# Kernel tuning notes

Hardware: AMD Instinct MI355X
Metric: run time of the kernel (lower is better)

The kernel has to match this reference:

```python
import jax, jax.numpy as jnp
import numpy as np

SAMPLE_POINTS = 1000
THRESH = 0.1
MAX_RATIO = 0.1
BIG = 1e9


def _sobel_boundary(mask):
    # mask: [B, H, W] -> boundary magnitude [B, H, W]
    kx = jnp.array([[-1, 0, 1], [-2, 0, 2], [-1, 0, 1]], jnp.float32).reshape(1, 1, 3, 3)
    ky = jnp.array([[-1, -2, -1], [0, 0, 0], [1, 2, 1]], jnp.float32).reshape(1, 1, 3, 3)
    x = mask[:, None, :, :]
    dn = ('NCHW', 'OIHW', 'NCHW')
    gx = jax.lax.conv_general_dilated(x, kx, (1, 1), [(1, 1), (1, 1)], dimension_numbers=dn)
    gy = jax.lax.conv_general_dilated(x, ky, (1, 1), [(1, 1), (1, 1)], dimension_numbers=dn)
    return jnp.sqrt(gx * gx + gy * gy + 1e-8)[:, 0]


def _extract_points(bmap, keys, H, W):
    # bmap: [B, H, W]. Returns points [B, P, 2] float and validity mask [B, P].
    # Torch version uses torch.where + randperm subsampling; here we pick a
    # uniformly-random subset of valid boundary pixels via noisy top_k
    # (fixed-shape, jit-compatible stream compaction).
    def one(bm, key):
        flat = bm.reshape(-1)
        valid = flat > THRESH
        noise = jax.random.uniform(key, flat.shape)
        score = valid.astype(jnp.float32) * 2.0 + noise  # valid in (2,3), invalid in (0,1)
        _, idx = jax.lax.top_k(score, SAMPLE_POINTS)
        pts = jnp.stack([(idx // W).astype(jnp.float32), (idx % W).astype(jnp.float32)], axis=-1)
        pvalid = valid[idx]
        has_any = valid.any()
        # empty-boundary fallback: single center point (like torch version)
        center = jnp.array([H // 2, W // 2], jnp.float32)
        pts = jnp.where(has_any, pts, jnp.broadcast_to(center, pts.shape))
        pvalid = jnp.where(has_any, pvalid, jnp.arange(SAMPLE_POINTS) == 0)
        return pts, pvalid

    return jax.vmap(one)(bmap, keys)


def _hausdorff(pp, pv, tp, tv, diag):
    # pp: [B,P,2], tp: [B,T,2]; masked symmetric Hausdorff per batch element.
    pp2 = jnp.sum(pp * pp, -1)  # [B,P]
    tp2 = jnp.sum(tp * tp, -1)  # [B,T]
    d2 = pp2[:, :, None] + tp2[:, None, :] - 2.0 * jnp.einsum('bpc,btc->bpt', pp, tp)
    D = jnp.sqrt(jnp.maximum(d2, 0.0))  # [B,P,T]
    min_p2t = jnp.min(jnp.where(tv[:, None, :], D, BIG), axis=2)  # [B,P]
    a = jnp.max(jnp.where(pv, min_p2t, -BIG), axis=1)  # [B]
    min_t2p = jnp.min(jnp.where(pv[:, :, None], D, BIG), axis=1)  # [B,T]
    b = jnp.max(jnp.where(tv, min_t2p, -BIG), axis=1)  # [B]
    hd = jnp.maximum(a, b) / diag
    return jnp.clip(hd, 0.0, MAX_RATIO)


def setup_inputs() -> dict:
    key = jax.random.key(0)
    k1, k2 = jax.random.split(key)
    B, H, W = 64, 512, 512
    pred_logits = jax.random.normal(k1, (B, H, W), dtype=jnp.float32)
    target = (jax.random.uniform(k2, (B, H, W)) > 0.5).astype(jnp.float32)
    return {"pred_logits": pred_logits, "target": target}


def reference(pred_logits, target):
    B, H, W = pred_logits.shape
    pred_probs = jax.nn.sigmoid(pred_logits)
    bmap_pred = _sobel_boundary(pred_probs)
    bmap_tgt = _sobel_boundary(target)
    keys = jax.random.split(jax.random.key(1), 2 * B)
    pp, pv = _extract_points(bmap_pred, keys[:B], H, W)
    tp, tv = _extract_points(bmap_tgt, keys[B:], H, W)
    diag = jnp.sqrt(jnp.float32(H * H + W * W))
    hd = _hausdorff(pp, pv, tp, tv, diag)  # [B]
    return jnp.mean(hd)
```

## Files before the change

### kernel.cpp

```cpp
#include <hip/hip_runtime.h>
#include <stdint.h>


#define HH 512
#define WW 512
#define NPIX (HH * WW)
#define NSEL 1000
#define SLICE_CAP 320
#define CUTM (253u << 14)
#define BITCUT ((((253u << 15) - 1u)) << 9)
#define ROWS_PER 32

#if __has_builtin(__builtin_amdgcn_alignbit)
__device__ __forceinline__ uint32_t rotl32(uint32_t x, int r) {
  return __builtin_amdgcn_alignbit(x, x, (32 - r) & 31);
}
#else
__device__ __forceinline__ uint32_t rotl32(uint32_t x, int r) {
  return (x << r) | (x >> (32 - r));
}
#endif

__device__ __forceinline__ void tf2x32(uint32_t k0, uint32_t k1,
                                       uint32_t c0, uint32_t c1,
                                       uint32_t& o0, uint32_t& o1) {
  uint32_t ks2 = k0 ^ k1 ^ 0x1BD11BDAu;
  uint32_t x0 = c0 + k0, x1 = c1 + k1;
#define TF_R(r) { x0 += x1; x1 = rotl32(x1, (r)); x1 ^= x0; }
  TF_R(13) TF_R(15) TF_R(26) TF_R(6)
  x0 += k1;  x1 += ks2 + 1u;
  TF_R(17) TF_R(29) TF_R(16) TF_R(24)
  x0 += ks2; x1 += k0 + 2u;
  TF_R(13) TF_R(15) TF_R(26) TF_R(6)
  x0 += k0;  x1 += k1 + 3u;
  TF_R(17) TF_R(29) TF_R(16) TF_R(24)
  x0 += k1;  x1 += ks2 + 4u;
  TF_R(13) TF_R(15) TF_R(26) TF_R(6)
  x0 += ks2; x1 += k0 + 5u;
#undef TF_R
  o0 = x0; o1 = x1;
}

__device__ __forceinline__ uint32_t tf_bits(uint32_t k0, uint32_t k1, uint32_t p) {
  uint32_t ks2 = k0 ^ k1 ^ 0x1BD11BDAu;
  uint32_t x0 = k0, x1 = p + k1;
#define TF_R(r) { x0 += x1; x1 = rotl32(x1, (r)); x1 ^= x0; }
  TF_R(13) TF_R(15) TF_R(26) TF_R(6)
  x0 += k1;  x1 += ks2 + 1u;
  TF_R(17) TF_R(29) TF_R(16) TF_R(24)
  x0 += ks2; x1 += k0 + 2u;
  TF_R(13) TF_R(15) TF_R(26) TF_R(6)
  x0 += k0;  x1 += k1 + 3u;
  TF_R(17) TF_R(29) TF_R(16) TF_R(24)
  x0 += k1;  x1 += ks2 + 4u;
  TF_R(13) TF_R(15) TF_R(26) TF_R(6)
  x0 += ks2; x1 += k0 + 5u;
#undef TF_R
  return x0 ^ x1;
}

__device__ __forceinline__ uint32_t m_from_bits(uint32_t bits) {
  float noise = __uint_as_float((bits >> 9) | 0x3F800000u) - 1.0f;
  float score = 2.0f + noise;
  return __float_as_uint(score) - 0x40000000u;
}

__device__ __forceinline__ uint32_t pixel_m(uint32_t k0, uint32_t k1, int p) {
  uint32_t b1, b2;
  tf2x32(k0, k1, 0u, (uint32_t)p, b1, b2);
  return m_from_bits(b1 ^ b2);
}

__device__ __forceinline__ float sigf(float x) { return 1.0f / (1.0f + __expf(-x)); }

__device__ __forceinline__ float ldval(const float* __restrict__ img, int r, int c, bool isPred) {
  if (r < 0 || r > HH - 1 || c < 0 || c > WW - 1) return 0.0f;
  float v = img[(size_t)r * WW + c];
  return isPred ? sigf(v) : v;
}

__device__ __forceinline__ uint32_t pack_pt(uint32_t p) {
  return ((p >> 9) << 16) | (p & 511u);
}

template <bool PRED>
__device__ __forceinline__ void sobel_body(const float* __restrict__ img, int b,
                                           int slice, int t,
                                           unsigned long long* stage, int* s_cn,
                                           int* s_cv) {
  const int lane = t & 63, w = t >> 6;
  const int rbase = slice * ROWS_PER + 8 * w;
  uint32_t k0, k1;
  tf2x32(0u, 1u, 0u, (uint32_t)b, k0, k1);
  k0 = __builtin_amdgcn_readfirstlane(k0);
  k1 = __builtin_amdgcn_readfirstlane(k1);

  float4 ra[3], rb[3];
  float v[3][10];
  int cnt = 0;
  const uint32_t pbase = (uint32_t)((rbase << 9) + (lane << 3));

  auto load_raw = [&](int s, int rn) {
    if ((unsigned)rn < (unsigned)HH) {
      const float* rp = img + ((size_t)rn << 9) + (lane << 3);
      ra[s] = *(const float4*)rp;
      rb[s] = *(const float4*)(rp + 4);
    }
  };
  auto promote = [&](int s, int rn) {
    float (&vv)[10] = v[s];
    if ((unsigned)rn < (unsigned)HH) {
      float4 x = ra[s], y = rb[s];
      if (PRED) {
        x.x = sigf(x.x); x.y = sigf(x.y); x.z = sigf(x.z); x.w = sigf(x.w);
        y.x = sigf(y.x); y.y = sigf(y.y); y.z = sigf(y.z); y.w = sigf(y.w);
      }
      vv[1] = x.x; vv[2] = x.y; vv[3] = x.z; vv[4] = x.w;
      vv[5] = y.x; vv[6] = y.y; vv[7] = y.z; vv[8] = y.w;
      float l = __shfl_up(y.w, 1);
      float r = __shfl_down(x.x, 1);
      vv[0] = (lane == 0) ? 0.0f : l;
      vv[9] = (lane == 63) ? 0.0f : r;
    } else {
#pragma unroll
      for (int i = 0; i < 10; ++i) vv[i] = 0.0f;
    }
  };

  load_raw(0, rbase - 1);
  load_raw(1, rbase);
  load_raw(2, rbase + 1);
  promote(0, rbase - 1);
  promote(1, rbase);

#pragma unroll
  for (int r = 0; r < 8; ++r) {
    load_raw(r % 3, rbase + r + 2);

    const uint32_t prow_r = pbase + (uint32_t)(r << 9);
    uint32_t bits[8];
#pragma unroll
    for (int j = 0; j < 8; ++j) bits[j] = tf_bits(k0, k1, prow_r + (uint32_t)j);

    promote((r + 2) % 3, rbase + r + 1);

    const int ip = r % 3, iq = (r + 1) % 3, ir = (r + 2) % 3;
    float da[10], e[10];
#pragma unroll
    for (int k = 0; k < 10; ++k) {
      da[k] = v[ir][k] - v[ip][k];
      e[k] = v[ip][k] + 2.0f * v[iq][k] + v[ir][k];
    }
    uint32_t candmask = 0;
#pragma unroll
    for (int j = 0; j < 8; ++j) {
      float gx = e[j + 2] - e[j];
      float gy = da[j] + 2.0f * da[j + 1] + da[j + 2];
      bool vld = (gx * gx + gy * gy + 1e-8f) > 0.01f;
      cnt += vld ? 1 : 0;
      candmask |= ((vld && bits[j] >= BITCUT) ? 1u : 0u) << j;
    }
    while (candmask) {
      int j = __ffs(candmask) - 1;
      candmask &= candmask - 1;
      uint32_t m = m_from_bits(bits[j]);
      int i = atomicAdd(s_cn, 1);
      if (i < SLICE_CAP)
        stage[i] = ((unsigned long long)m << 32) | (prow_r + (uint32_t)j);
    }
  }
#pragma unroll
  for (int o = 32; o > 0; o >>= 1) cnt += __shfl_down(cnt, o);
  if (lane == 0) atomicAdd(s_cv, cnt);
}

__global__ __launch_bounds__(256, 4) void sobel_cand(
    const float* __restrict__ pred, const float* __restrict__ tgt,
    int2* __restrict__ g_scnt, unsigned long long* __restrict__ g_cand) {
  const int bid = blockIdx.x;
  const int b = bid >> 4, s = bid & 15;
  const int t = threadIdx.x;
  __shared__ unsigned long long stage[SLICE_CAP];
  __shared__ int s_cn, s_cv;
  if (t == 0) { s_cn = 0; s_cv = 0; }
  __syncthreads();
  if (b < 64) sobel_body<true>(pred + (size_t)b * NPIX, b, s, t, stage, &s_cn, &s_cv);
  else        sobel_body<false>(tgt + (size_t)(b - 64) * NPIX, b, s, t, stage, &s_cn, &s_cv);
  __syncthreads();
  const int raw = s_cn;
  const int n = raw < SLICE_CAP ? raw : SLICE_CAP;
  for (int i = t; i < n; i += 256) g_cand[(size_t)bid * SLICE_CAP + i] = stage[i];
  if (t == 0) g_scnt[bid] = make_int2(s_cv, raw);
}

__global__ __launch_bounds__(256) void resolve_kernel(
    const float* __restrict__ pred, const float* __restrict__ tgt,
    const int2* __restrict__ g_scnt, unsigned long long* __restrict__ g_cand,
    uint32_t* __restrict__ g_pts, int* __restrict__ g_counts) {
  const int img = blockIdx.x;
  const int t = threadIdx.x;

  __shared__ int segc[16];
  __shared__ int s_info[4];
  __shared__ int ch[256];
  __shared__ int fh[1024];
  __shared__ int aux[256];
  __shared__ unsigned long long ties[256];
  __shared__ int s_pos, s_nt, s_T1, s_r1, s_T2, s_r2;

  if (t == 0) {
    int cv = 0, hi = 0, ovf = 0;
    for (int s = 0; s < 16; ++s) {
      int2 v = g_scnt[img * 16 + s];
      cv += v.x;
      hi += v.y;
      segc[s] = v.y < SLICE_CAP ? v.y : SLICE_CAP;
      if (v.y > SLICE_CAP) ovf = 1;
    }
    s_info[0] = cv; s_info[1] = hi; s_info[2] = ovf;
    s_pos = 0; s_nt = 0;
  }
  __syncthreads();
  const int cv = s_info[0];
  if (cv == 0) {
    if (t == 0) { g_pts[img * NSEL] = (256u << 16) | 256u; g_counts[img] = 1; }
    return;
  }
  const int need = cv < NSEL ? cv : NSEL;
  bool slow = (s_info[2] != 0) || (s_info[1] < need);

  unsigned long long* C = g_cand + (size_t)img * 16 * SLICE_CAP;
  int ncand;

  if (slow) {
    const bool isPred = img < 64;
    const float* im = isPred ? pred + (size_t)img * NPIX : tgt + (size_t)(img - 64) * NPIX;
    uint32_t k0, k1;
    tf2x32(0u, 1u, 0u, (uint32_t)img, k0, k1);
    ch[t] = 0;
    __syncthreads();
    for (int p = t; p < NPIX; p += 256) {
      int r = p >> 9, c = p & 511;
      float gx = (ldval(im, r - 1, c + 1, isPred) - ldval(im, r - 1, c - 1, isPred)) +
                 2.0f * (ldval(im, r, c + 1, isPred) - ldval(im, r, c - 1, isPred)) +
                 (ldval(im, r + 1, c + 1, isPred) - ldval(im, r + 1, c - 1, isPred));
      float gy = (ldval(im, r + 1, c - 1, isPred) - ldval(im, r - 1, c - 1, isPred)) +
                 2.0f * (ldval(im, r + 1, c, isPred) - ldval(im, r - 1, c, isPred)) +
                 (ldval(im, r + 1, c + 1, isPred) - ldval(im, r - 1, c + 1, isPred));
      if ((gx * gx + gy * gy + 1e-8f) > 0.01f) {
        uint32_t m = pixel_m(k0, k1, p);
        uint32_t cb = m >> 14; if (cb > 255u) cb = 255u;
        atomicAdd(&ch[cb], 1);
      }
    }
    __syncthreads();
    {
      aux[t] = ch[t];
      __syncthreads();
      for (int o = 1; o < 256; o <<= 1) {
        int v = (t + o < 256) ? aux[t + o] : 0;
        __syncthreads();
        aux[t] += v;
        __syncthreads();
      }
      int nx = (t + 1 < 256) ? aux[t + 1] : 0;
      if (aux[t] >= need && nx < need) s_T1 = t;
      __syncthreads();
    }
    const uint32_t Tc = (uint32_t)s_T1;
    if (t == 0) s_info[3] = 0;
    __syncthreads();
    for (int p = t; p < NPIX; p += 256) {
      int r = p >> 9, c = p & 511;
      float gx = (ldval(im, r - 1, c + 1, isPred) - ldval(im, r - 1, c - 1, isPred)) +
                 2.0f * (ldval(im, r, c + 1, isPred) - ldval(im, r, c - 1, isPred)) +
                 (ldval(im, r + 1, c + 1, isPred) - ldval(im, r + 1, c - 1, isPred));
      float gy = (ldval(im, r + 1, c - 1, isPred) - ldval(im, r - 1, c - 1, isPred)) +
                 2.0f * (ldval(im, r + 1, c, isPred) - ldval(im, r - 1, c, isPred)) +
                 (ldval(im, r + 1, c + 1, isPred) - ldval(im, r - 1, c + 1, isPred));
      if ((gx * gx + gy * gy + 1e-8f) > 0.01f) {
        uint32_t m = pixel_m(k0, k1, p);
        uint32_t cb = m >> 14; if (cb > 255u) cb = 255u;
        if (cb >= Tc) {
          int i = atomicAdd(&s_info[3], 1);
          if (i < 16 * SLICE_CAP) C[i] = ((unsigned long long)m << 32) | (uint32_t)p;
        }
      }
    }
    __syncthreads();
    ncand = s_info[3] < 16 * SLICE_CAP ? s_info[3] : 16 * SLICE_CAP;
    if (t == 0) { segc[0] = ncand; for (int s = 1; s < 16; ++s) segc[s] = 0; }
    __syncthreads();
  }

  ch[t] = 0;
  for (int i = t; i < 1024; i += 256) fh[i] = 0;
  __syncthreads();
  for (int s = 0; s < 16; ++s) {
    const unsigned long long* seg = C + (size_t)s * SLICE_CAP;
    for (int i = t; i < segc[s]; i += 256) {
      uint32_t m = (uint32_t)(seg[i] >> 32);
      uint32_t cb = m >> 14; if (cb > 255u) cb = 255u;
      atomicAdd(&ch[cb], 1);
    }
  }
  __syncthreads();
  {
    aux[t] = ch[t];
    __syncthreads();
    for (int o = 1; o < 256; o <<= 1) {
      int v = (t + o < 256) ? aux[t + o] : 0;
      __syncthreads();
      aux[t] += v;
      __syncthreads();
    }
    int nx = (t + 1 < 256) ? aux[t + 1] : 0;
    if (aux[t] >= need && nx < need) { s_T1 = t; s_r1 = need - nx; }
    __syncthreads();
  }
  const uint32_t T1 = (uint32_t)s_T1;
  const int r1 = s_r1;
  const uint32_t baseM = T1 << 14;

  for (int s = 0; s < 16; ++s) {
    const unsigned long long* seg = C + (size_t)s * SLICE_CAP;
    for (int i = t; i < segc[s]; i += 256) {
      unsigned long long e = seg[i];
      uint32_t m = (uint32_t)(e >> 32), p = (uint32_t)e;
      uint32_t cb = m >> 14; if (cb > 255u) cb = 255u;
      if (cb > T1) {
        int pos = atomicAdd(&s_pos, 1);
        g_pts[img * NSEL + pos] = pack_pt(p);
      } else if (cb == T1) {
        uint32_t f = (m - baseM) >> 4; if (f > 1023u) f = 1023u;
        atomicAdd(&fh[f], 1);
      }
    }
  }
  __syncthreads();
  {
    int base = 4 * t, sv = 0;
    for (int j = 3; j >= 0; --j) { sv += fh[base + j]; fh[base + j] = sv; }
    aux[t] = sv;
    __syncthreads();
    for (int o = 1; o < 256; o <<= 1) {
      int v = (t + o < 256) ? aux[t + o] : 0;
      __syncthreads();
      aux[t] += v;
      __syncthreads();
    }
    int add = (t < 255) ? aux[t + 1] : 0;
    for (int j = 0; j < 4; ++j) fh[base + j] += add;
    __syncthreads();
    for (int j = 0; j < 4; ++j) {
      int idx = base + j;
      int sfx = fh[idx];
      int nx = (idx < 1023) ? fh[idx + 1] : 0;
      if (sfx >= r1 && nx < r1) { s_T2 = idx; s_r2 = r1 - nx; }
    }
    __syncthreads();
  }
  const int T2 = s_T2, r2 = s_r2;
  for (int s = 0; s < 16; ++s) {
    const unsigned long long* seg = C + (size_t)s * SLICE_CAP;
    for (int i = t; i < segc[s]; i += 256) {
      unsigned long long e = seg[i];
      uint32_t m = (uint32_t)(e >> 32), p = (uint32_t)e;
      uint32_t cb = m >> 14; if (cb > 255u) cb = 255u;
      if (cb == T1) {
        uint32_t f = (m - baseM) >> 4; if (f > 1023u) f = 1023u;
        if ((int)f > T2) {
          int pos = atomicAdd(&s_pos, 1);
          g_pts[img * NSEL + pos] = pack_pt(p);
        } else if ((int)f == T2) {
          int j = atomicAdd(&s_nt, 1);
          if (j < 256) ties[j] = e;
        }
      }
    }
  }
  __syncthreads();
  int nt = s_nt < 256 ? s_nt : 256;
  for (int i = t; i < nt; i += 256) {
    unsigned long long e = ties[i];
    uint32_t mi = (uint32_t)(e >> 32), pi = (uint32_t)e;
    int rank = 0;
    for (int j = 0; j < nt; ++j) {
      unsigned long long e2 = ties[j];
      uint32_t mj = (uint32_t)(e2 >> 32), pj = (uint32_t)e2;
      rank += (mj > mi) || (mj == mi && pj < pi);
    }
    if (rank < r2) {
      int pos = atomicAdd(&s_pos, 1);
      g_pts[img * NSEL + pos] = pack_pt(pi);
    }
  }
  __syncthreads();
  if (t == 0) g_counts[img] = s_pos;
}

__global__ __launch_bounds__(256) void haus_kernel(
    const uint32_t* __restrict__ g_pts, const int* __restrict__ g_counts,
    float* __restrict__ g_hpart) {
  const int bid = blockIdx.x;
  const int img = bid >> 3;
  const int dir = (bid >> 2) & 1;
  const int seg = bid & 3;
  const int t = threadIdx.x;
  const int iOwn = dir ? 64 + img : img;
  const int iOth = dir ? img : 64 + img;
  const int nOwn = g_counts[iOwn];
  const int nOth = g_counts[iOth];
  __shared__ float2 o[NSEL];
  __shared__ float red[256];
  for (int i = t; i < nOth; i += 256) {
    uint32_t v = g_pts[iOth * NSEL + i];
    o[i] = make_float2((float)(v >> 16), (float)(v & 0xFFFFu));
  }
  __syncthreads();
  float best = 0.0f;
  const int lo = seg * 250;
  const int hi = min(nOwn, lo + 250);
  for (int i = lo + t; i < hi; i += 256) {
    uint32_t v = g_pts[iOwn * NSEL + i];
    float pr = (float)(v >> 16), pc = (float)(v & 0xFFFFu);
    float mn0 = 3.4e38f, mn1 = 3.4e38f, mn2 = 3.4e38f, mn3 = 3.4e38f;
    int j = 0;
    for (; j + 3 < nOth; j += 4) {
      float dr0 = pr - o[j].x,     dc0 = pc - o[j].y;
      float dr1 = pr - o[j + 1].x, dc1 = pc - o[j + 1].y;
      float dr2 = pr - o[j + 2].x, dc2 = pc - o[j + 2].y;
      float dr3 = pr - o[j + 3].x, dc3 = pc - o[j + 3].y;
      mn0 = fminf(mn0, dr0 * dr0 + dc0 * dc0);
      mn1 = fminf(mn1, dr1 * dr1 + dc1 * dc1);
      mn2 = fminf(mn2, dr2 * dr2 + dc2 * dc2);
      mn3 = fminf(mn3, dr3 * dr3 + dc3 * dc3);
    }
    for (; j < nOth; ++j) {
      float dr = pr - o[j].x, dc = pc - o[j].y;
      mn0 = fminf(mn0, dr * dr + dc * dc);
    }
    float mn = fminf(fminf(mn0, mn1), fminf(mn2, mn3));
    best = fmaxf(best, mn);
  }
  red[t] = best;
  __syncthreads();
  for (int st = 128; st > 0; st >>= 1) {
    if (t < st) red[t] = fmaxf(red[t], red[t + st]);
    __syncthreads();
  }
  if (t == 0) g_hpart[bid] = red[0];
}

__global__ __launch_bounds__(64) void fin_kernel(const float* __restrict__ g_hpart,
                                                 float* __restrict__ out) {
  const int t = threadIdx.x;
  float mx = 0.0f;
  for (int j = 0; j < 8; ++j) mx = fmaxf(mx, g_hpart[t * 8 + j]);
  float diag = sqrtf((float)(HH * HH + WW * WW));
  float hd = sqrtf(fmaxf(mx, 0.0f)) / diag;
  hd = fminf(fmaxf(hd, 0.0f), 0.1f);
  float s = hd;
  for (int o = 32; o > 0; o >>= 1) s += __shfl_down(s, o);
  if (t == 0) out[0] = s * 0.015625f;
}

#define WS_SCNT   0u
#define WS_COUNTS 16384u
#define WS_HPART  (WS_COUNTS + 512u)
#define WS_PTS    (WS_HPART + 2048u)
#define WS_CAND   (WS_PTS + 512000u)

extern "C" void kernel_launch(void* const* d_in, const int* in_sizes, int n_in,
                              void* d_out, int out_size, void* d_ws, size_t ws_size,
                              hipStream_t stream) {
  const float* pred = (const float*)d_in[0];
  const float* tgt = (const float*)d_in[1];
  float* out = (float*)d_out;
  char* ws = (char*)d_ws;
  int2* g_scnt = (int2*)(ws + WS_SCNT);
  int* g_counts = (int*)(ws + WS_COUNTS);
  float* g_hpart = (float*)(ws + WS_HPART);
  uint32_t* g_pts = (uint32_t*)(ws + WS_PTS);
  unsigned long long* g_cand = (unsigned long long*)(ws + WS_CAND);

  sobel_cand<<<2048, 256, 0, stream>>>(pred, tgt, g_scnt, g_cand);
  resolve_kernel<<<128, 256, 0, stream>>>(pred, tgt, g_scnt, g_cand, g_pts, g_counts);
  haus_kernel<<<512, 256, 0, stream>>>(g_pts, g_counts, g_hpart);
  fin_kernel<<<1, 64, 0, stream>>>(g_hpart, out);
}
```

Before: 243.9 us.

## Stage candidates in LDS for resolve and reroll Sobel row loop

```diff
diff --git a/kernel.cpp b/kernel.cpp
--- a/kernel.cpp
+++ b/kernel.cpp
@@ -95,22 +95,21 @@
   k0 = __builtin_amdgcn_readfirstlane(k0);
   k1 = __builtin_amdgcn_readfirstlane(k1);
 
-  float4 ra[3], rb[3];
-  float v[3][10];
+  float P[10], Q[10], R[10];
+  float4 na, nb;
   int cnt = 0;
   const uint32_t pbase = (uint32_t)((rbase << 9) + (lane << 3));
 
-  auto load_raw = [&](int s, int rn) {
+  auto issue = [&](int rn) {
     if ((unsigned)rn < (unsigned)HH) {
       const float* rp = img + ((size_t)rn << 9) + (lane << 3);
-      ra[s] = *(const float4*)rp;
-      rb[s] = *(const float4*)(rp + 4);
+      na = *(const float4*)rp;
+      nb = *(const float4*)(rp + 4);
     }
   };
-  auto promote = [&](int s, int rn) {
-    float (&vv)[10] = v[s];
+  auto promote = [&](float (&vv)[10], int rn) {
     if ((unsigned)rn < (unsigned)HH) {
-      float4 x = ra[s], y = rb[s];
+      float4 x = na, y = nb;
       if (PRED) {
         x.x = sigf(x.x); x.y = sigf(x.y); x.z = sigf(x.z); x.w = sigf(x.w);
         y.x = sigf(y.x); y.y = sigf(y.y); y.z = sigf(y.z); y.w = sigf(y.w);
@@ -127,29 +126,26 @@
     }
   };
 
-  load_raw(0, rbase - 1);
-  load_raw(1, rbase);
-  load_raw(2, rbase + 1);
-  promote(0, rbase - 1);
-  promote(1, rbase);
-
-#pragma unroll
+  issue(rbase - 1); promote(P, rbase - 1);
+  issue(rbase);     promote(Q, rbase);
+  issue(rbase + 1);
+
+#pragma unroll 1
   for (int r = 0; r < 8; ++r) {
-    load_raw(r % 3, rbase + r + 2);
-
-    const uint32_t prow_r = pbase + (uint32_t)(r << 9);
+    promote(R, rbase + r + 1);
+    if (r < 7) issue(rbase + r + 2);
+    __builtin_amdgcn_sched_barrier(0);
+
+    const uint32_t prow = pbase + ((uint32_t)r << 9);
     uint32_t bits[8];
 #pragma unroll
-    for (int j = 0; j < 8; ++j) bits[j] = tf_bits(k0, k1, prow_r + (uint32_t)j);
-
-    promote((r + 2) % 3, rbase + r + 1);
-
-    const int ip = r % 3, iq = (r + 1) % 3, ir = (r + 2) % 3;
+    for (int j = 0; j < 8; ++j) bits[j] = tf_bits(k0, k1, prow + (uint32_t)j);
+
     float da[10], e[10];
 #pragma unroll
     for (int k = 0; k < 10; ++k) {
-      da[k] = v[ir][k] - v[ip][k];
-      e[k] = v[ip][k] + 2.0f * v[iq][k] + v[ir][k];
+      da[k] = R[k] - P[k];
+      e[k] = P[k] + 2.0f * Q[k] + R[k];
     }
     uint32_t candmask = 0;
 #pragma unroll
@@ -166,8 +162,10 @@
       uint32_t m = m_from_bits(bits[j]);
       int i = atomicAdd(s_cn, 1);
       if (i < SLICE_CAP)
-        stage[i] = ((unsigned long long)m << 32) | (prow_r + (uint32_t)j);
-    }
+        stage[i] = ((unsigned long long)m << 32) | (prow + (uint32_t)j);
+    }
+#pragma unroll
+    for (int k = 0; k < 10; ++k) { P[k] = Q[k]; Q[k] = R[k]; }
   }
 #pragma unroll
   for (int o = 32; o > 0; o >>= 1) cnt += __shfl_down(cnt, o);
@@ -200,25 +198,30 @@
   const int img = blockIdx.x;
   const int t = threadIdx.x;
 
+  __shared__ unsigned long long cand_s[16 * SLICE_CAP];
   __shared__ int segc[16];
+  __shared__ int s_scx[16], s_scy[16];
   __shared__ int s_info[4];
   __shared__ int ch[256];
   __shared__ int fh[1024];
   __shared__ int aux[256];
   __shared__ unsigned long long ties[256];
-  __shared__ int s_pos, s_nt, s_T1, s_r1, s_T2, s_r2;
-
+  __shared__ int s_pos, s_nt, s_T1, s_r1, s_T2, s_r2, s_n;
+
+  if (t < 16) {
+    int2 v = g_scnt[img * 16 + t];
+    s_scx[t] = v.x; s_scy[t] = v.y;
+    segc[t] = v.y < SLICE_CAP ? v.y : SLICE_CAP;
+  }
+  if (t == 0) { s_pos = 0; s_nt = 0; s_n = 0; }
+  __syncthreads();
   if (t == 0) {
     int cv = 0, hi = 0, ovf = 0;
     for (int s = 0; s < 16; ++s) {
-      int2 v = g_scnt[img * 16 + s];
-      cv += v.x;
-      hi += v.y;
-      segc[s] = v.y < SLICE_CAP ? v.y : SLICE_CAP;
-      if (v.y > SLICE_CAP) ovf = 1;
+      cv += s_scx[s]; hi += s_scy[s];
+      if (s_scy[s] > SLICE_CAP) ovf = 1;
     }
     s_info[0] = cv; s_info[1] = hi; s_info[2] = ovf;
-    s_pos = 0; s_nt = 0;
   }
   __syncthreads();
   const int cv = s_info[0];
@@ -230,7 +233,7 @@
   bool slow = (s_info[2] != 0) || (s_info[1] < need);
 
   unsigned long long* C = g_cand + (size_t)img * 16 * SLICE_CAP;
-  int ncand;
+  int ncand = 0;
 
   if (slow) {
     const bool isPred = img < 64;
@@ -289,20 +292,30 @@
     }
     __syncthreads();
     ncand = s_info[3] < 16 * SLICE_CAP ? s_info[3] : 16 * SLICE_CAP;
-    if (t == 0) { segc[0] = ncand; for (int s = 1; s < 16; ++s) segc[s] = 0; }
-    __syncthreads();
-  }
-
+  }
+
+  if (slow) {
+    for (int i = t; i < ncand; i += 256) cand_s[i] = C[i];
+    if (t == 0) s_n = ncand;
+  } else {
+    for (int i = t; i < 16 * SLICE_CAP; i += 256) {
+      int s = i / SLICE_CAP;
+      int o = i - s * SLICE_CAP;
+      if (o < segc[s]) {
+        unsigned long long e = C[i];
+        cand_s[atomicAdd(&s_n, 1)] = e;
+      }
+    }
+  }
   ch[t] = 0;
   for (int i = t; i < 1024; i += 256) fh[i] = 0;
   __syncthreads();
-  for (int s = 0; s < 16; ++s) {
-    const unsigned long long* seg = C + (size_t)s * SLICE_CAP;
-    for (int i = t; i < segc[s]; i += 256) {
-      uint32_t m = (uint32_t)(seg[i] >> 32);
-      uint32_t cb = m >> 14; if (cb > 255u) cb = 255u;
-      atomicAdd(&ch[cb], 1);
-    }
+  const int n = s_n;
+
+  for (int i = t; i < n; i += 256) {
+    uint32_t m = (uint32_t)(cand_s[i] >> 32);
+    uint32_t cb = m >> 14; if (cb > 255u) cb = 255u;
+    atomicAdd(&ch[cb], 1);
   }
   __syncthreads();
   {
@@ -322,19 +335,16 @@
   const int r1 = s_r1;
   const uint32_t baseM = T1 << 14;
 
-  for (int s = 0; s < 16; ++s) {
-    const unsigned long long* seg = C + (size_t)s * SLICE_CAP;
-    for (int i = t; i < segc[s]; i += 256) {
-      unsigned long long e = seg[i];
-      uint32_t m = (uint32_t)(e >> 32), p = (uint32_t)e;
-      uint32_t cb = m >> 14; if (cb > 255u) cb = 255u;
-      if (cb > T1) {
-        int pos = atomicAdd(&s_pos, 1);
-        g_pts[img * NSEL + pos] = pack_pt(p);
-      } else if (cb == T1) {
-        uint32_t f = (m - baseM) >> 4; if (f > 1023u) f = 1023u;
-        atomicAdd(&fh[f], 1);
-      }
+  for (int i = t; i < n; i += 256) {
+    unsigned long long e = cand_s[i];
+    uint32_t m = (uint32_t)(e >> 32), p = (uint32_t)e;
+    uint32_t cb = m >> 14; if (cb > 255u) cb = 255u;
+    if (cb > T1) {
+      int pos = atomicAdd(&s_pos, 1);
+      g_pts[img * NSEL + pos] = pack_pt(p);
+    } else if (cb == T1) {
+      uint32_t f = (m - baseM) >> 4; if (f > 1023u) f = 1023u;
+      atomicAdd(&fh[f], 1);
     }
   }
   __syncthreads();
@@ -361,21 +371,18 @@
     __syncthreads();
   }
   const int T2 = s_T2, r2 = s_r2;
-  for (int s = 0; s < 16; ++s) {
-    const unsigned long long* seg = C + (size_t)s * SLICE_CAP;
-    for (int i = t; i < segc[s]; i += 256) {
-      unsigned long long e = seg[i];
-      uint32_t m = (uint32_t)(e >> 32), p = (uint32_t)e;
-      uint32_t cb = m >> 14; if (cb > 255u) cb = 255u;
-      if (cb == T1) {
-        uint32_t f = (m - baseM) >> 4; if (f > 1023u) f = 1023u;
-        if ((int)f > T2) {
-          int pos = atomicAdd(&s_pos, 1);
-          g_pts[img * NSEL + pos] = pack_pt(p);
-        } else if ((int)f == T2) {
-          int j = atomicAdd(&s_nt, 1);
-          if (j < 256) ties[j] = e;
-        }
+  for (int i = t; i < n; i += 256) {
+    unsigned long long e = cand_s[i];
+    uint32_t m = (uint32_t)(e >> 32), p = (uint32_t)e;
+    uint32_t cb = m >> 14; if (cb > 255u) cb = 255u;
+    if (cb == T1) {
+      uint32_t f = (m - baseM) >> 4; if (f > 1023u) f = 1023u;
+      if ((int)f > T2) {
+        int pos = atomicAdd(&s_pos, 1);
+        g_pts[img * NSEL + pos] = pack_pt(p);
+      } else if ((int)f == T2) {
+        int j = atomicAdd(&s_nt, 1);
+        if (j < 256) ties[j] = e;
       }
     }
   }
```

Result: faster. 234.3 us (-4.0%).
